# Performance work log

Measured on AMD Instinct MI355X. Metric: run time of the kernel, lower is better.

The kernel has to match this reference:

```python
import jax, jax.numpy as jnp
import numpy as np

NUM_HEADS = 4
NUM_GROUPS = 8
EPS = 1e-5


def setup_inputs() -> dict:
    key = jax.random.key(0)
    ks = jax.random.split(key, 4)
    b, c, h, w = 16, 512, 32, 32
    x = jax.random.normal(ks[0], (b, c, h, w), dtype=jnp.float32)
    gamma = jnp.ones((c,), dtype=jnp.float32)
    beta = jnp.zeros((c,), dtype=jnp.float32)
    # conv1d kernel-size-1 weights expressed as [out, in] matrices
    w_qkv = jax.random.normal(ks[1], (3 * c, c), dtype=jnp.float32) * (1.0 / np.sqrt(c))
    b_qkv = jnp.zeros((3 * c,), dtype=jnp.float32)
    w_proj = jax.random.normal(ks[2], (c, c), dtype=jnp.float32) * (1.0 / np.sqrt(c))
    b_proj = jnp.zeros((c,), dtype=jnp.float32)
    return {"x": x, "gamma": gamma, "beta": beta, "w_qkv": w_qkv,
            "b_qkv": b_qkv, "w_proj": w_proj, "b_proj": b_proj}


def group_norm(x, gamma, beta):
    # x: [b, c, h, w]; normalize per (group) over (c/g, h, w)
    b, c, h, w = x.shape
    xg = x.reshape(b, NUM_GROUPS, c // NUM_GROUPS, h, w)
    mean = xg.mean(axis=(2, 3, 4), keepdims=True)
    var = xg.var(axis=(2, 3, 4), keepdims=True)
    xn = ((xg - mean) * jax.lax.rsqrt(var + EPS)).reshape(b, c, h, w)
    return xn * gamma[None, :, None, None] + beta[None, :, None, None]


def reference(x, gamma, beta, w_qkv, b_qkv, w_proj, b_proj):
    b, c, h, w = x.shape
    L = h * w
    hd = c // NUM_HEADS  # head_dim
    x_in = x
    xn = group_norm(x, gamma, beta).reshape(b, c, L)
    # 1x1 conv == matmul over channel dim: [b, 3c, L]
    qkv = jnp.einsum('oc,bcl->bol', w_qkv, xn) + b_qkv[None, :, None]
    q, k, v = jnp.split(qkv, 3, axis=1)  # each [b, c, L]
    q = q.reshape(b, NUM_HEADS, hd, L)
    k = k.reshape(b, NUM_HEADS, hd, L)
    v = v.reshape(b, NUM_HEADS, hd, L)
    scale = hd ** (-0.5)
    attn = jnp.einsum('bhdl,bhdm->bhlm', q * scale, k)  # [b,h,L,L]
    attn = jax.nn.softmax(attn, axis=-1)
    out = jnp.einsum('bhlm,bhdm->bhdl', attn, v).reshape(b, c, L)
    out = jnp.einsum('oc,bcl->bol', w_proj, out) + b_proj[None, :, None]
    return x_in + out.reshape(b, c, h, w)
```

## Files before the change

kernel.cpp:

```cpp
#include <hip/hip_runtime.h>
#include <hip/hip_bf16.h>

typedef __hip_bfloat16 bf16;
typedef __attribute__((ext_vector_type(8))) short short8;
typedef __attribute__((ext_vector_type(4))) float f32x4;
typedef __attribute__((ext_vector_type(16))) float f32x16;

__device__ __forceinline__ float b2f(bf16 v) { return __bfloat162float(v); }
__device__ __forceinline__ bf16  f2b(float v) { return __float2bfloat16(v); }

__device__ __forceinline__ unsigned cvt_pk_bf16(float lo, float hi) {
    unsigned r;
    asm("v_cvt_pk_bf16_f32 %0, %1, %2" : "=v"(r) : "v"(lo), "v"(hi));
    return r;
}

__global__ __launch_bounds__(256) void convert_w_kernel(
    const float* __restrict__ wq, const float* __restrict__ wp,
    bf16* __restrict__ wqb, bf16* __restrict__ wpb)
{
    int ch = blockIdx.x * 256 + threadIdx.x;
    float4 v;
    bf16* dst;
    if (ch < 196608) {
        v = ((const float4*)wq)[ch];
        dst = wqb + ch * 4;
    } else {
        int c2 = ch - 196608;
        v = ((const float4*)wp)[c2];
        dst = wpb + c2 * 4;
    }
    bf16 o[4] = {f2b(v.x), f2b(v.y), f2b(v.z), f2b(v.w)};
    *(uint2*)dst = *(const uint2*)o;
}

__global__ __launch_bounds__(256) void gn_partial_kernel(
    const float* __restrict__ x,
    float* __restrict__ partS, float* __restrict__ partQ)
{
    const int bid = blockIdx.x;
    const size_t base = (size_t)bid * 16384;
    const int t = threadIdx.x;

    float sum = 0.f, ssq = 0.f;
    const float4* x4 = (const float4*)(x + base);
    for (int i = t; i < 4096; i += 256) {
        float4 v = x4[i];
        sum += v.x + v.y + v.z + v.w;
        ssq += v.x * v.x + v.y * v.y + v.z * v.z + v.w * v.w;
    }
    #pragma unroll
    for (int off = 32; off > 0; off >>= 1) {
        sum += __shfl_down(sum, off);
        ssq += __shfl_down(ssq, off);
    }
    __shared__ float red[8];
    const int wid = t >> 6, lane = t & 63;
    if (lane == 0) { red[wid] = sum; red[4 + wid] = ssq; }
    __syncthreads();
    if (t == 0) {
        partS[bid] = red[0] + red[1] + red[2] + red[3];
        partQ[bid] = red[4] + red[5] + red[6] + red[7];
    }
}

__global__ __launch_bounds__(64) void gn_finalize_kernel(
    const float* __restrict__ partS, const float* __restrict__ partQ,
    const float* __restrict__ gamma, const float* __restrict__ beta,
    float* __restrict__ scaleB, float* __restrict__ shiftB)
{
    const int bg = blockIdx.x;
    const int b = bg >> 3, g = bg & 7;
    const int t = threadIdx.x;
    float s = partS[bg * 4] + partS[bg * 4 + 1] + partS[bg * 4 + 2] + partS[bg * 4 + 3];
    float q = partQ[bg * 4] + partQ[bg * 4 + 1] + partQ[bg * 4 + 2] + partQ[bg * 4 + 3];
    float mean = s * (1.f / 65536.f);
    float var  = q * (1.f / 65536.f) - mean * mean;
    float rstd = rsqrtf(var + 1e-5f);
    int c = g * 64 + t;
    float sc = rstd * gamma[c];
    scaleB[b * 512 + c] = sc;
    shiftB[b * 512 + c] = beta[c] - mean * sc;
}

__global__ __launch_bounds__(256) void gn_apply_t_kernel(
    const float* __restrict__ x,
    const float* __restrict__ scaleB,
    const float* __restrict__ shiftB,
    bf16* __restrict__ Xt)
{
    const int lt = blockIdx.x, ct = blockIdx.y, b = blockIdx.z;
    const int l0 = lt * 64, c0 = ct * 64;
    const int t = threadIdx.x;
    __shared__ float Ls[64][65];

    const float* xb = x + ((size_t)b * 512 + c0) * 1024 + l0;
    for (int i = t; i < 1024; i += 256) {
        int cc = i >> 4, lc = (i & 15) * 4;
        float4 v = *(const float4*)(xb + (size_t)cc * 1024 + lc);
        float sc = scaleB[b * 512 + c0 + cc];
        float sh = shiftB[b * 512 + c0 + cc];
        Ls[cc][lc]     = v.x * sc + sh;
        Ls[cc][lc + 1] = v.y * sc + sh;
        Ls[cc][lc + 2] = v.z * sc + sh;
        Ls[cc][lc + 3] = v.w * sc + sh;
    }
    __syncthreads();
    for (int i = t; i < 1024; i += 256) {
        int l = i >> 4, cc = (i & 15) * 4;
        bf16 o[4] = {f2b(Ls[cc][l]), f2b(Ls[cc + 1][l]),
                     f2b(Ls[cc + 2][l]), f2b(Ls[cc + 3][l])};
        *(uint2*)(Xt + ((size_t)b * 1024 + l0 + l) * 512 + c0 + cc) = *(const uint2*)o;
    }
}

__global__ __launch_bounds__(256) void mfma_qkv_kernel(
    const bf16* __restrict__ W,
    const bf16* __restrict__ Xt,
    const float* __restrict__ bias,
    bf16* __restrict__ Qt,
    bf16* __restrict__ Kt,
    bf16* __restrict__ Vb)
{
    const int n0 = blockIdx.x * 128;
    const int m0 = blockIdx.y * 128;
    const int b  = blockIdx.z;
    const int t  = threadIdx.x;
    const int w  = t >> 6, lane = t & 63;
    const int c  = lane & 15, quad = lane >> 4;
    const int w0 = w & 1, w1 = w >> 1;
    const int ak = quad * 8;

    __shared__ __align__(16) bf16 smem[17408];
    bf16* As = smem;
    bf16* Bs = smem + 5120;
    bf16* Cs = smem;

    const bf16* Ag = W + (size_t)m0 * 512;
    const bf16* Bg = Xt + ((size_t)b * 1024 + n0) * 512;

    const int srow = t >> 2, skc = (t & 3) * 8;

    short8 areg[2], breg[2];
    #pragma unroll
    for (int it = 0; it < 2; it++) {
        int row = srow + it * 64;
        areg[it] = *(const short8*)(Ag + (size_t)row * 512 + skc);
        breg[it] = *(const short8*)(Bg + (size_t)row * 512 + skc);
    }

    f32x4 acc[4][4];
    #pragma unroll
    for (int i = 0; i < 4; i++)
        #pragma unroll
        for (int j = 0; j < 4; j++)
            #pragma unroll
            for (int r = 0; r < 4; r++) acc[i][j][r] = 0.f;

    for (int k0 = 0; k0 < 512; k0 += 32) {
        __syncthreads();
        #pragma unroll
        for (int it = 0; it < 2; it++) {
            int row = srow + it * 64;
            *(short8*)&As[row * 40 + skc] = areg[it];
            *(short8*)&Bs[row * 40 + skc] = breg[it];
        }
        __syncthreads();
        {
            int k1 = (k0 + 32) & 511;
            #pragma unroll
            for (int it = 0; it < 2; it++) {
                int row = srow + it * 64;
                areg[it] = *(const short8*)(Ag + (size_t)row * 512 + k1 + skc);
                breg[it] = *(const short8*)(Bg + (size_t)row * 512 + k1 + skc);
            }
        }
        short8 af[4], bf[4];
        #pragma unroll
        for (int jm = 0; jm < 4; jm++)
            af[jm] = *(const short8*)&As[(w0 * 64 + jm * 16 + c) * 40 + ak];
        #pragma unroll
        for (int jn = 0; jn < 4; jn++)
            bf[jn] = *(const short8*)&Bs[(w1 * 64 + jn * 16 + c) * 40 + ak];
        #pragma unroll
        for (int jm = 0; jm < 4; jm++)
            #pragma unroll
            for (int jn = 0; jn < 4; jn++)
                acc[jm][jn] = __builtin_amdgcn_mfma_f32_16x16x32_bf16(
                    af[jm], bf[jn], acc[jm][jn], 0, 0, 0);
    }

    __syncthreads();
    const int cls = m0 >> 9;
    if (cls < 2) {
        #pragma unroll
        for (int jm = 0; jm < 4; jm++) {
            #pragma unroll
            for (int jn = 0; jn < 4; jn++) {
                bf16 o4[4];
                #pragma unroll
                for (int r = 0; r < 4; r++) {
                    int orow = w0 * 64 + jm * 16 + quad * 4 + r;
                    o4[r] = f2b(acc[jm][jn][r] + bias[m0 + orow]);
                }
                *(uint2*)&Cs[(size_t)(w1 * 64 + jn * 16 + c) * 136
                             + w0 * 64 + jm * 16 + quad * 4] = *(const uint2*)o4;
            }
        }
        __syncthreads();
        const int head = (m0 >> 7) & 3;
        bf16* Db = (cls == 0 ? Qt : Kt)
                   + (((size_t)(b * 4 + head)) * 1024 + n0) * 128;
        for (int i = t; i < 2048; i += 256) {
            int row = i >> 4, ch = (i & 15) * 8;
            *(short8*)(Db + (size_t)row * 128 + ch) = *(const short8*)&Cs[row * 136 + ch];
        }
    } else {
        #pragma unroll
        for (int jm = 0; jm < 4; jm++) {
            #pragma unroll
            for (int r = 0; r < 4; r++) {
                int orow = w0 * 64 + jm * 16 + quad * 4 + r;
                float bs = bias[m0 + orow];
                #pragma unroll
                for (int jn = 0; jn < 4; jn++)
                    Cs[orow * 136 + w1 * 64 + jn * 16 + c] = f2b(acc[jm][jn][r] + bs);
            }
        }
        __syncthreads();
        bf16* Cb = Vb + ((size_t)b * 512 + (m0 - 1024)) * 1024 + n0;
        for (int i = t; i < 2048; i += 256) {
            int row = i >> 4, ch = (i & 15) * 8;
            *(short8*)(Cb + (size_t)row * 1024 + ch) = *(const short8*)&Cs[row * 136 + ch];
        }
    }
}

#define HD 128
#define QT 128
#define MT 64

__global__ __launch_bounds__(256, 2) void attn_mfma_kernel(
    const bf16* __restrict__ Qt,
    const bf16* __restrict__ Kt,
    const bf16* __restrict__ Vb,
    bf16* __restrict__ out)
{
    const int bh = blockIdx.x;
    const int qt = blockIdx.y;
    const int b = bh >> 2, h = bh & 3;
    const int t = threadIdx.x;
    const int w = t >> 6, lane = t & 63;
    const int wrow = lane & 31;
    const int blk  = lane >> 5;
    const int l0 = qt * QT;

    __shared__ __align__(16) bf16 smem[2 * 17920];

    const int qrow = w * 32 + wrow;
    const bf16* Qr = Qt + (((size_t)(b * 4 + h)) * 1024 + l0 + qrow) * 128;
    short8 aq[8];
    #pragma unroll
    for (int kt = 0; kt < 8; kt++)
        aq[kt] = *(const short8*)(Qr + kt * 16 + blk * 8);

    const bf16* Kb = Kt + (((size_t)(b * 4 + h)) * 1024) * 128;
    const bf16* Vg = Vb + ((size_t)(b * 512 + h * HD)) * 1024;

    short8 kreg[4], vreg[4];
    #pragma unroll
    for (int p = 0; p < 4; p++) {
        int i = t + p * 256;
        kreg[p] = *(const short8*)(Kb + (size_t)(i >> 4) * 128 + (i & 15) * 8);
        vreg[p] = *(const short8*)(Vg + (size_t)(i >> 3) * 1024 + (i & 7) * 8);
    }

    f32x16 acc_o[4];
    #pragma unroll
    for (int n = 0; n < 4; n++)
        #pragma unroll
        for (int r = 0; r < 16; r++) acc_o[n][r] = 0.f;

    float psl4[4] = {0.f, 0.f, 0.f, 0.f};

    const float kSc = 0.08838834764831845f * 1.4426950408889634f;
    const float kSh = 6.0f * 1.4426950408889634f;

    for (int mt = 0; mt < 1024 / MT; mt++) {
        bf16* Ks = smem + (mt & 1) * 17920;
        bf16* Vs = Ks + 8704;

        #pragma unroll
        for (int p = 0; p < 4; p++) {
            int i = t + p * 256;
            int m = i >> 4;
            int mrow = (m & 51) | ((m & 4) << 1) | ((m & 8) >> 1);
            *(short8*)&Ks[mrow * 136 + (i & 15) * 8] = kreg[p];
            *(short8*)&Vs[(i >> 3) * 72 + (i & 7) * 8]  = vreg[p];
        }
        __syncthreads();

        {
            int m0n = (mt < 15) ? (mt + 1) * MT : 0;
            #pragma unroll
            for (int p = 0; p < 4; p++) {
                int i = t + p * 256;
                kreg[p] = *(const short8*)(Kb + (size_t)(m0n + (i >> 4)) * 128 + (i & 15) * 8);
                vreg[p] = *(const short8*)(Vg + (size_t)(i >> 3) * 1024 + m0n + (i & 7) * 8);
            }
        }

        f32x16 accs[2];
        #pragma unroll
        for (int n = 0; n < 2; n++)
            #pragma unroll
            for (int r = 0; r < 16; r++) accs[n][r] = 0.f;
        __builtin_amdgcn_s_setprio(1);
        #pragma unroll
        for (int kt = 0; kt < 8; kt++) {
            #pragma unroll
            for (int nt = 0; nt < 2; nt++) {
                short8 afr = *(const short8*)&Ks[(nt * 32 + wrow) * 136 + kt * 16 + blk * 8];
                accs[nt] = __builtin_amdgcn_mfma_f32_32x32x16_bf16(afr, aq[kt], accs[nt], 0, 0, 0);
            }
        }
        __builtin_amdgcn_s_setprio(0);

        unsigned pw[2][8];
        #pragma unroll
        for (int nt = 0; nt < 2; nt++) {
            float pv[16];
            #pragma unroll
            for (int r = 0; r < 16; r++)
                pv[r] = exp2f(accs[nt][r] * kSc - kSh);
            #pragma unroll
            for (int r = 0; r < 16; r++) psl4[r & 3] += pv[r];
            #pragma unroll
            for (int wd = 0; wd < 8; wd++)
                pw[nt][wd] = cvt_pk_bf16(pv[2 * wd], pv[2 * wd + 1]);
        }

        __builtin_amdgcn_s_setprio(1);
        #pragma unroll
        for (int kt2 = 0; kt2 < 4; kt2++) {
            union { short8 s; unsigned u[4]; } pa;
            #pragma unroll
            for (int wd = 0; wd < 4; wd++)
                pa.u[wd] = pw[kt2 >> 1][(kt2 & 1) * 4 + wd];
            #pragma unroll
            for (int nt2 = 0; nt2 < 4; nt2++) {
                short8 bv = *(const short8*)&Vs[(nt2 * 32 + wrow) * 72 + kt2 * 16 + blk * 8];
                acc_o[nt2] = __builtin_amdgcn_mfma_f32_32x32x16_bf16(pa.s, bv, acc_o[nt2], 0, 0, 0);
            }
        }
        __builtin_amdgcn_s_setprio(0);
    }

    float psl = (psl4[0] + psl4[1]) + (psl4[2] + psl4[3]);
    float tot = psl + __shfl_xor(psl, 32);
    float inv[16];
    #pragma unroll
    for (int r = 0; r < 16; r++) {
        int q = (r & 3) + 8 * (r >> 2) + 4 * blk;
        inv[r] = __builtin_amdgcn_rcpf(__shfl(tot, q | (lane & 32)));
    }

    bf16* Os = smem;
    #pragma unroll
    for (int nt2 = 0; nt2 < 4; nt2++)
        #pragma unroll
        for (int r = 0; r < 16; r++) {
            int row = w * 32 + (r & 3) + 8 * (r >> 2) + 4 * blk;
            Os[row * 136 + nt2 * 32 + wrow] = f2b(acc_o[nt2][r] * inv[r]);
        }
    __syncthreads();
    bf16* Ob = out + ((size_t)b * 1024 + l0) * 512 + h * HD;
    for (int i = t; i < 2048; i += 256) {
        int row = i >> 4, ch = (i & 15) * 8;
        *(short8*)(Ob + (size_t)row * 512 + ch) = *(const short8*)&Os[row * 136 + ch];
    }
}

__global__ __launch_bounds__(256) void mfma_proj_kernel(
    const bf16* __restrict__ W,
    const bf16* __restrict__ Xt,
    const float* __restrict__ bias,
    const float* __restrict__ res,
    float* __restrict__ C)
{
    const int n0 = blockIdx.x * 128;
    const int m0 = blockIdx.y * 128;
    const int b  = blockIdx.z;
    const int t  = threadIdx.x;
    const int w  = t >> 6, lane = t & 63;
    const int c  = lane & 15, quad = lane >> 4;
    const int w0 = w & 1, w1 = w >> 1;
    const int ak = quad * 8;

    __shared__ __align__(16) bf16 smem[17408];
    bf16* As = smem;
    bf16* Bs = smem + 5120;
    bf16* Cs = smem;

    const bf16* Ag = W + (size_t)m0 * 512;
    const bf16* Bg = Xt + ((size_t)b * 1024 + n0) * 512;

    const int srow = t >> 2, skc = (t & 3) * 8;

    short8 areg[2], breg[2];
    #pragma unroll
    for (int it = 0; it < 2; it++) {
        int row = srow + it * 64;
        areg[it] = *(const short8*)(Ag + (size_t)row * 512 + skc);
        breg[it] = *(const short8*)(Bg + (size_t)row * 512 + skc);
    }

    f32x4 acc[4][4];
    #pragma unroll
    for (int i = 0; i < 4; i++)
        #pragma unroll
        for (int j = 0; j < 4; j++)
            #pragma unroll
            for (int r = 0; r < 4; r++) acc[i][j][r] = 0.f;

    for (int k0 = 0; k0 < 512; k0 += 32) {
        __syncthreads();
        #pragma unroll
        for (int it = 0; it < 2; it++) {
            int row = srow + it * 64;
            *(short8*)&As[row * 40 + skc] = areg[it];
            *(short8*)&Bs[row * 40 + skc] = breg[it];
        }
        __syncthreads();
        {
            int k1 = (k0 + 32) & 511;
            #pragma unroll
            for (int it = 0; it < 2; it++) {
                int row = srow + it * 64;
                areg[it] = *(const short8*)(Ag + (size_t)row * 512 + k1 + skc);
                breg[it] = *(const short8*)(Bg + (size_t)row * 512 + k1 + skc);
            }
        }
        short8 af[4], bf[4];
        #pragma unroll
        for (int jm = 0; jm < 4; jm++)
            af[jm] = *(const short8*)&As[(w0 * 64 + jm * 16 + c) * 40 + ak];
        #pragma unroll
        for (int jn = 0; jn < 4; jn++)
            bf[jn] = *(const short8*)&Bs[(w1 * 64 + jn * 16 + c) * 40 + ak];
        #pragma unroll
        for (int jm = 0; jm < 4; jm++)
            #pragma unroll
            for (int jn = 0; jn < 4; jn++)
                acc[jm][jn] = __builtin_amdgcn_mfma_f32_16x16x32_bf16(
                    af[jm], bf[jn], acc[jm][jn], 0, 0, 0);
    }

    __syncthreads();
    #pragma unroll
    for (int jm = 0; jm < 4; jm++) {
        #pragma unroll
        for (int r = 0; r < 4; r++) {
            int orow = w0 * 64 + jm * 16 + quad * 4 + r;
            float bs = bias[m0 + orow];
            #pragma unroll
            for (int jn = 0; jn < 4; jn++)
                Cs[orow * 136 + w1 * 64 + jn * 16 + c] = f2b(acc[jm][jn][r] + bs);
        }
    }
    __syncthreads();
    const float* Rb = res + ((size_t)b * 512 + m0) * 1024 + n0;
    float* Cb = C + ((size_t)b * 512 + m0) * 1024 + n0;
    for (int i = t; i < 4096; i += 256) {
        int row = i >> 5, ch = (i & 31) * 4;
        float4 rv = *(const float4*)(Rb + (size_t)row * 1024 + ch);
        float4 ov;
        ov.x = b2f(Cs[row * 136 + ch + 0]) + rv.x;
        ov.y = b2f(Cs[row * 136 + ch + 1]) + rv.y;
        ov.z = b2f(Cs[row * 136 + ch + 2]) + rv.z;
        ov.w = b2f(Cs[row * 136 + ch + 3]) + rv.w;
        *(float4*)(Cb + (size_t)row * 1024 + ch) = ov;
    }
}

extern "C" void kernel_launch(void* const* d_in, const int* in_sizes, int n_in,
                              void* d_out, int out_size, void* d_ws, size_t ws_size,
                              hipStream_t stream)
{
    const float* x      = (const float*)d_in[0];
    const float* gamma  = (const float*)d_in[1];
    const float* beta   = (const float*)d_in[2];
    const float* w_qkv  = (const float*)d_in[3];
    const float* b_qkv  = (const float*)d_in[4];
    const float* w_proj = (const float*)d_in[5];
    const float* b_proj = (const float*)d_in[6];
    float* out = (float*)d_out;

    char* ws = (char*)d_ws;
    float* scaleB = (float*)ws;
    float* shiftB = (float*)(ws + 32768);
    bf16*  wqb    = (bf16*)(ws + 65536);
    bf16*  wpb    = (bf16*)(ws + 65536 + 1572864);
    char*  big    = ws + 65536 + 2097152;
    bf16*  Xt     = (bf16*)(big);
    bf16*  Qt     = (bf16*)(big + (size_t)16777216);
    bf16*  Kt     = (bf16*)(big + (size_t)2 * 16777216);
    bf16*  Vb     = (bf16*)(big + (size_t)3 * 16777216);
    float* partS  = (float*)(big + (size_t)4 * 16777216);
    float* partQ  = partS + 512;
    bf16*  attn_t = Xt;

    hipLaunchKernelGGL(convert_w_kernel, dim3(1024), dim3(256), 0, stream,
                       w_qkv, w_proj, wqb, wpb);
    hipLaunchKernelGGL(gn_partial_kernel, dim3(512), dim3(256), 0, stream,
                       x, partS, partQ);
    hipLaunchKernelGGL(gn_finalize_kernel, dim3(128), dim3(64), 0, stream,
                       partS, partQ, gamma, beta, scaleB, shiftB);
    hipLaunchKernelGGL(gn_apply_t_kernel, dim3(16, 8, 16), dim3(256), 0, stream,
                       x, scaleB, shiftB, Xt);
    hipLaunchKernelGGL(mfma_qkv_kernel, dim3(8, 12, 16), dim3(256), 0, stream,
                       wqb, Xt, b_qkv, Qt, Kt, Vb);
    hipLaunchKernelGGL(attn_mfma_kernel, dim3(64, 8), dim3(256), 0, stream,
                       Qt, Kt, Vb, attn_t);
    hipLaunchKernelGGL(mfma_proj_kernel, dim3(8, 4, 16), dim3(256), 0, stream,
                       wpb, attn_t, b_proj, x, out);
}
```

Baseline: 226.5 us.

## Split attention KV tile across two wave groups with LDS reduction

Doubles the attention block to 512 threads (8 waves) and gives each pair of waves the same 32 query rows but a different 32-column half of each 64-key tile. The partial P·V accumulators and row sums from the two halves are combined through shared memory at the end before normalization. The aim is more waves in flight to hide latency and fewer registers per wave, at the cost of an extra fp32 reduction through LDS and more barriers. The fixed-shift exp without a running max is unchanged.

```diff
diff --git a/kernel.cpp b/kernel.cpp
--- a/kernel.cpp
+++ b/kernel.cpp
@@ -240,7 +240,7 @@
 #define QT 128
 #define MT 64
 
-__global__ __launch_bounds__(256, 2) void attn_mfma_kernel(
+__global__ __launch_bounds__(512, 4) void attn_mfma_kernel(
     const bf16* __restrict__ Qt,
     const bf16* __restrict__ Kt,
     const bf16* __restrict__ Vb,
@@ -253,11 +253,13 @@
     const int w = t >> 6, lane = t & 63;
     const int wrow = lane & 31;
     const int blk  = lane >> 5;
+    const int qsub = w & 3;
+    const int msub = w >> 2;
     const int l0 = qt * QT;
 
     __shared__ __align__(16) bf16 smem[2 * 17920];
 
-    const int qrow = w * 32 + wrow;
+    const int qrow = qsub * 32 + wrow;
     const bf16* Qr = Qt + (((size_t)(b * 4 + h)) * 1024 + l0 + qrow) * 128;
     short8 aq[8];
     #pragma unroll
@@ -267,10 +269,10 @@
     const bf16* Kb = Kt + (((size_t)(b * 4 + h)) * 1024) * 128;
     const bf16* Vg = Vb + ((size_t)(b * 512 + h * HD)) * 1024;
 
-    short8 kreg[4], vreg[4];
-    #pragma unroll
-    for (int p = 0; p < 4; p++) {
-        int i = t + p * 256;
+    short8 kreg[2], vreg[2];
+    #pragma unroll
+    for (int p = 0; p < 2; p++) {
+        int i = t + p * 512;
         kreg[p] = *(const short8*)(Kb + (size_t)(i >> 4) * 128 + (i & 15) * 8);
         vreg[p] = *(const short8*)(Vg + (size_t)(i >> 3) * 1024 + (i & 7) * 8);
     }
@@ -291,8 +293,8 @@
         bf16* Vs = Ks + 8704;
 
         #pragma unroll
-        for (int p = 0; p < 4; p++) {
-            int i = t + p * 256;
+        for (int p = 0; p < 2; p++) {
+            int i = t + p * 512;
             int m = i >> 4;
             int mrow = (m & 51) | ((m & 4) << 1) | ((m & 8) >> 1);
             *(short8*)&Ks[mrow * 136 + (i & 15) * 8] = kreg[p];
@@ -303,53 +305,46 @@
         {
             int m0n = (mt < 15) ? (mt + 1) * MT : 0;
             #pragma unroll
-            for (int p = 0; p < 4; p++) {
-                int i = t + p * 256;
+            for (int p = 0; p < 2; p++) {
+                int i = t + p * 512;
                 kreg[p] = *(const short8*)(Kb + (size_t)(m0n + (i >> 4)) * 128 + (i & 15) * 8);
                 vreg[p] = *(const short8*)(Vg + (size_t)(i >> 3) * 1024 + m0n + (i & 7) * 8);
             }
         }
 
-        f32x16 accs[2];
-        #pragma unroll
-        for (int n = 0; n < 2; n++)
-            #pragma unroll
-            for (int r = 0; r < 16; r++) accs[n][r] = 0.f;
+        f32x16 accs;
+        #pragma unroll
+        for (int r = 0; r < 16; r++) accs[r] = 0.f;
         __builtin_amdgcn_s_setprio(1);
         #pragma unroll
         for (int kt = 0; kt < 8; kt++) {
-            #pragma unroll
-            for (int nt = 0; nt < 2; nt++) {
-                short8 afr = *(const short8*)&Ks[(nt * 32 + wrow) * 136 + kt * 16 + blk * 8];
-                accs[nt] = __builtin_amdgcn_mfma_f32_32x32x16_bf16(afr, aq[kt], accs[nt], 0, 0, 0);
-            }
+            short8 afr = *(const short8*)&Ks[(msub * 32 + wrow) * 136 + kt * 16 + blk * 8];
+            accs = __builtin_amdgcn_mfma_f32_32x32x16_bf16(afr, aq[kt], accs, 0, 0, 0);
         }
         __builtin_amdgcn_s_setprio(0);
 
-        unsigned pw[2][8];
-        #pragma unroll
-        for (int nt = 0; nt < 2; nt++) {
-            float pv[16];
-            #pragma unroll
-            for (int r = 0; r < 16; r++)
-                pv[r] = exp2f(accs[nt][r] * kSc - kSh);
-            #pragma unroll
-            for (int r = 0; r < 16; r++) psl4[r & 3] += pv[r];
-            #pragma unroll
-            for (int wd = 0; wd < 8; wd++)
-                pw[nt][wd] = cvt_pk_bf16(pv[2 * wd], pv[2 * wd + 1]);
-        }
+        float pv[16];
+        #pragma unroll
+        for (int r = 0; r < 16; r++)
+            pv[r] = exp2f(accs[r] * kSc - kSh);
+        #pragma unroll
+        for (int r = 0; r < 16; r++) psl4[r & 3] += pv[r];
+        unsigned pw[8];
+        #pragma unroll
+        for (int wd = 0; wd < 8; wd++)
+            pw[wd] = cvt_pk_bf16(pv[2 * wd], pv[2 * wd + 1]);
 
         __builtin_amdgcn_s_setprio(1);
         #pragma unroll
-        for (int kt2 = 0; kt2 < 4; kt2++) {
+        for (int kt2 = 0; kt2 < 2; kt2++) {
             union { short8 s; unsigned u[4]; } pa;
             #pragma unroll
             for (int wd = 0; wd < 4; wd++)
-                pa.u[wd] = pw[kt2 >> 1][(kt2 & 1) * 4 + wd];
+                pa.u[wd] = pw[kt2 * 4 + wd];
             #pragma unroll
             for (int nt2 = 0; nt2 < 4; nt2++) {
-                short8 bv = *(const short8*)&Vs[(nt2 * 32 + wrow) * 72 + kt2 * 16 + blk * 8];
+                short8 bv = *(const short8*)&Vs[(nt2 * 32 + wrow) * 72
+                                                + msub * 32 + kt2 * 16 + blk * 8];
                 acc_o[nt2] = __builtin_amdgcn_mfma_f32_32x32x16_bf16(pa.s, bv, acc_o[nt2], 0, 0, 0);
             }
         }
@@ -358,24 +353,55 @@
 
     float psl = (psl4[0] + psl4[1]) + (psl4[2] + psl4[3]);
     float tot = psl + __shfl_xor(psl, 32);
-    float inv[16];
-    #pragma unroll
-    for (int r = 0; r < 16; r++) {
-        int q = (r & 3) + 8 * (r >> 2) + 4 * blk;
-        inv[r] = __builtin_amdgcn_rcpf(__shfl(tot, q | (lane & 32)));
-    }
-
+    __syncthreads();
+
+    float* F   = (float*)smem;
+    float* psr = F + 128 * 130;
+    psr[w * 32 + wrow] = tot;
+    if (msub == 0) {
+        #pragma unroll
+        for (int nt2 = 0; nt2 < 4; nt2++)
+            #pragma unroll
+            for (int r = 0; r < 16; r++) {
+                int q = qsub * 32 + (r & 3) + 8 * (r >> 2) + 4 * blk;
+                F[q * 130 + nt2 * 32 + wrow] = acc_o[nt2][r];
+            }
+    }
+    __syncthreads();
+    if (msub == 1) {
+        float tot_all = psr[w * 32 + wrow] + psr[(w ^ 4) * 32 + wrow];
+        #pragma unroll
+        for (int nt2 = 0; nt2 < 4; nt2++)
+            #pragma unroll
+            for (int r = 0; r < 16; r++) {
+                int q = qsub * 32 + (r & 3) + 8 * (r >> 2) + 4 * blk;
+                acc_o[nt2][r] += F[q * 130 + nt2 * 32 + wrow];
+            }
+        float inv[16];
+        #pragma unroll
+        for (int r = 0; r < 16; r++) {
+            int rm = (r & 3) + 8 * (r >> 2) + 4 * blk;
+            inv[r] = __builtin_amdgcn_rcpf(__shfl(tot_all, rm | (lane & 32)));
+        }
+        #pragma unroll
+        for (int nt2 = 0; nt2 < 4; nt2++)
+            #pragma unroll
+            for (int r = 0; r < 16; r++) acc_o[nt2][r] *= inv[r];
+    }
+    __syncthreads();
     bf16* Os = smem;
-    #pragma unroll
-    for (int nt2 = 0; nt2 < 4; nt2++)
-        #pragma unroll
-        for (int r = 0; r < 16; r++) {
-            int row = w * 32 + (r & 3) + 8 * (r >> 2) + 4 * blk;
-            Os[row * 136 + nt2 * 32 + wrow] = f2b(acc_o[nt2][r] * inv[r]);
-        }
+    if (msub == 1) {
+        #pragma unroll
+        for (int nt2 = 0; nt2 < 4; nt2++)
+            #pragma unroll
+            for (int r = 0; r < 16; r++) {
+                int q = qsub * 32 + (r & 3) + 8 * (r >> 2) + 4 * blk;
+                Os[q * 136 + nt2 * 32 + wrow] = f2b(acc_o[nt2][r]);
+            }
+    }
     __syncthreads();
     bf16* Ob = out + ((size_t)b * 1024 + l0) * 512 + h * HD;
-    for (int i = t; i < 2048; i += 256) {
+    for (int i = t; i < 2048; i += 512) {
         int row = i >> 4, ch = (i & 15) * 8;
         *(short8*)(Ob + (size_t)row * 512 + ch) = *(const short8*)&Os[row * 136 + ch];
     }
@@ -520,7 +546,7 @@
                        x, scaleB, shiftB, Xt);
     hipLaunchKernelGGL(mfma_qkv_kernel, dim3(8, 12, 16), dim3(256), 0, stream,
                        wqb, Xt, b_qkv, Qt, Kt, Vb);
-    hipLaunchKernelGGL(attn_mfma_kernel, dim3(64, 8), dim3(256), 0, stream,
+    hipLaunchKernelGGL(attn_mfma_kernel, dim3(64, 8), dim3(512), 0, stream,
                        Qt, Kt, Vb, attn_t);
     hipLaunchKernelGGL(mfma_proj_kernel, dim3(8, 4, 16), dim3(256), 0, stream,
                        wpb, attn_t, b_proj, x, out);
```

Result: slower. 287.3 us (+26.9%).
